# Optimization experiments

Hardware: AMD Instinct MI355X
Metric: run time of the kernel (lower is better)

Reference implementation:

```python
import jax, jax.numpy as jnp
import numpy as np

WINDOWS = (5, 10, 20)
EPS = 1e-4
K_SLICES = 3
OVERLAP = 0.5


def setup_inputs() -> dict:
    key = jax.random.key(0)
    k1, k2, k3, k4 = jax.random.split(key, 4)
    B, T, H = 64, 2048, 256
    x = jax.random.normal(k1, (B, T, H), dtype=jnp.float32)
    alpha = 0.1 * jax.random.normal(k2, (H, len(WINDOWS)), dtype=jnp.float32)
    gamma = 1.0 + 0.1 * jax.random.normal(k3, (K_SLICES, H), dtype=jnp.float32)
    beta = 0.1 * jax.random.normal(k4, (K_SLICES, H), dtype=jnp.float32)
    return {"x": x, "alpha": alpha, "gamma": gamma, "beta": beta}


def _fan(x, alpha):
    # FrequencyAdaptiveNormSimple: multi-window sliding mean/std, blended by softmax(alpha).
    B, T, H = x.shape
    al = jax.nn.softmax(alpha, axis=-1)  # [H, nW]
    # prefix sums for O(T) sliding statistics (same math as unfold mean/std)
    zrow = jnp.zeros((B, 1, H), x.dtype)
    S1 = jnp.concatenate([zrow, jnp.cumsum(x, axis=1)], axis=1)        # [B, T+1, H]
    S2 = jnp.concatenate([zrow, jnp.cumsum(x * x, axis=1)], axis=1)    # [B, T+1, H]
    out = jnp.zeros_like(x)
    for wi, w in enumerate(WINDOWS):
        if w > T:
            continue
        ws = S1[:, w:, :] - S1[:, : T - w + 1, :]    # window sums, [B, T-w+1, H]
        ws2 = S2[:, w:, :] - S2[:, : T - w + 1, :]
        mu = ws / w
        var = jnp.maximum((ws2 - ws * ws / w) / (w - 1), 0.0)  # unbiased (torch std default)
        sd = jnp.maximum(jnp.sqrt(var), EPS)
        # F.pad(..., (w-1, 0), mode='replicate') on the time dim
        mu = jnp.pad(mu, ((0, 0), (w - 1, 0), (0, 0)), mode="edge")
        sd = jnp.pad(sd, ((0, 0), (w - 1, 0), (0, 0)), mode="edge")
        z = jnp.nan_to_num((x - mu) / sd, nan=0.0, posinf=0.0, neginf=0.0)
        out = out + z * al[:, wi][None, None, :]
    return out


def _san(x, gamma, beta):
    # SliceAdaptiveNormSimple: overlapping slices, per-slice (B,T) stats (detached), affine, avg.
    B, T, H = x.shape
    step = max(1, int(round(T / (K_SLICES - (K_SLICES - 1) * OVERLAP))))
    win = min(T, step + int(round(step * OVERLAP)))
    y = jnp.zeros_like(x)
    cnt = jnp.zeros((B, T, 1), x.dtype)
    s = 0
    for k in range(K_SLICES):
        e = min(T, s + win)
        if e <= s:
            break
        xk = x[:, s:e, :]
        mu = jax.lax.stop_gradient(jnp.mean(xk, axis=(0, 1), keepdims=True))
        sd = jax.lax.stop_gradient(
            jnp.maximum(jnp.std(xk, axis=(0, 1), ddof=1, keepdims=True), 1e-4)
        )
        z = jnp.nan_to_num((xk - mu) / sd, nan=0.0, posinf=0.0, neginf=0.0)
        z = z * gamma[k][None, None, :] + beta[k][None, None, :]
        y = y.at[:, s:e, :].add(z)
        cnt = cnt.at[:, s:e, :].add(1.0)
        s += step
    return y / (cnt + EPS)


def reference(x, alpha, gamma, beta):
    # StableFANSAN: out = x + SAN(FAN(x))
    return x + _san(_fan(x, alpha), gamma, beta)
```

## Files before the change

kernel.cpp:

```cpp
#include <hip/hip_runtime.h>
#include <hip/hip_fp16.h>

#define T_DIM 2048
#define H_DIM 256
#define B_DIM 64

#define FCH 64
#define FNCH (T_DIM / FCH)
#define FNCB (B_DIM * FNCH)

#define ECH 64
#define ENCH (T_DIM / ECH)
#define ENCB (B_DIM * ENCH)

#define EPS_F 1e-4f
#define R1 (1.0f / 1.0001f)
#define R2 (1.0f / 2.0001f)

__device__ __forceinline__ void win_stats(float s1, float s2, float inv_w, float inv_wm1,
                                          float& mu, float& isd) {
    mu = s1 * inv_w;
    float var = fmaxf((s2 - s1 * s1 * inv_w) * inv_wm1, 0.0f);
    isd = fminf(rsqrtf(var), 1e4f);
}

template <int MODE, bool FIRST>
__device__ __forceinline__ void run_chunk(
    const float* __restrict__ xbh, __half* __restrict__ s16bh, float* __restrict__ s32bh,
    int t0, float al0, float al1, float al2,
    float& ls1, float& ls2,
    float mu5i, float isd5i, float mu10i, float isd10i, float mu20i, float isd20i) {

    float s1_5 = 0.f, s2_5 = 0.f, s1_10 = 0.f, s2_10 = 0.f, s1_20 = 0.f, s2_20 = 0.f;

    if (!FIRST) {
#pragma unroll
        for (int j = 1; j <= 20; ++j) {
            float v = xbh[(t0 - j) * H_DIM];
            s1_20 += v; s2_20 += v * v;
            if (j <= 10) { s1_10 += v; s2_10 += v * v; }
            if (j <= 5)  { s1_5  += v; s2_5  += v * v; }
        }
    }

    for (int i0 = 0; i0 < FCH; i0 += 32) {
#pragma unroll
        for (int k = 0; k < 32; ++k) {
            const int t = t0 + i0 + k;
            const float v = xbh[t * H_DIM];
            s1_5  += v; s2_5  += v * v;
            s1_10 += v; s2_10 += v * v;
            s1_20 += v; s2_20 += v * v;
            if (!FIRST || i0 + k >= 5)  { float o = xbh[(t - 5)  * H_DIM]; s1_5  -= o; s2_5  -= o * o; }
            if (!FIRST || i0 + k >= 10) { float o = xbh[(t - 10) * H_DIM]; s1_10 -= o; s2_10 -= o * o; }
            if (!FIRST || i0 + k >= 20) { float o = xbh[(t - 20) * H_DIM]; s1_20 -= o; s2_20 -= o * o; }

            float mu, isd, fan = 0.0f;
            if (!FIRST || i0 + k >= 4)  win_stats(s1_5,  s2_5,  0.2f,  0.25f,      mu, isd);
            else { mu = mu5i;  isd = isd5i; }
            fan += (v - mu) * isd * al0;
            if (!FIRST || i0 + k >= 9)  win_stats(s1_10, s2_10, 0.1f,  1.f / 9.f,  mu, isd);
            else { mu = mu10i; isd = isd10i; }
            fan += (v - mu) * isd * al1;
            if (!FIRST || i0 + k >= 19) win_stats(s1_20, s2_20, 0.05f, 1.f / 19.f, mu, isd);
            else { mu = mu20i; isd = isd20i; }
            fan += (v - mu) * isd * al2;

            ls1 += fan; ls2 += fan * fan;
            if (MODE == 0) s16bh[t * H_DIM] = __float2half(fan);
            else           s32bh[t * H_DIM] = fan;
        }
    }
}

template <int MODE>
__global__ __launch_bounds__(256, 4)
void fan_kernel(const float* __restrict__ x, const float* __restrict__ alpha,
                float* __restrict__ part, __half* __restrict__ stash16,
                float* __restrict__ stash32) {
    const int blk = (blockIdx.x & 7) * (FNCB / 8) + (blockIdx.x >> 3);
    const int b = blk / FNCH;
    const int c = blk % FNCH;
    const int h = threadIdx.x;
    const int t0 = c * FCH;
    const size_t base = (size_t)b * T_DIM * H_DIM + h;
    const float* xbh = x + base;
    __half* s16bh = (MODE == 0) ? stash16 + base : nullptr;
    float*  s32bh = (MODE == 1) ? stash32 + base : nullptr;

    const float a0 = alpha[h * 3 + 0], a1 = alpha[h * 3 + 1], a2 = alpha[h * 3 + 2];
    const float mx = fmaxf(a0, fmaxf(a1, a2));
    const float e0 = __expf(a0 - mx), e1 = __expf(a1 - mx), e2 = __expf(a2 - mx);
    const float einv = 1.0f / (e0 + e1 + e2);
    const float al0 = e0 * einv, al1 = e1 * einv, al2 = e2 * einv;

    float ls1 = 0.0f, ls2 = 0.0f;

    if (c == 0) {
        float mu5i, isd5i, mu10i, isd10i, mu20i, isd20i;
        float c1 = 0.f, c2 = 0.f;
#pragma unroll
        for (int j = 0; j < 20; ++j) {
            float v = xbh[j * H_DIM];
            c1 += v; c2 += v * v;
            if (j == 4)  win_stats(c1, c2, 0.2f,  0.25f,      mu5i,  isd5i);
            if (j == 9)  win_stats(c1, c2, 0.1f,  1.f / 9.f,  mu10i, isd10i);
            if (j == 19) win_stats(c1, c2, 0.05f, 1.f / 19.f, mu20i, isd20i);
        }
        run_chunk<MODE, true>(xbh, s16bh, s32bh, t0, al0, al1, al2, ls1, ls2,
                              mu5i, isd5i, mu10i, isd10i, mu20i, isd20i);
    } else {
        run_chunk<MODE, false>(xbh, s16bh, s32bh, t0, al0, al1, al2, ls1, ls2,
                               0.f, 0.f, 0.f, 0.f, 0.f, 0.f);
    }

    part[(0 * FNCB + blk) * H_DIM + h] = ls1;
    part[(1 * FNCB + blk) * H_DIM + h] = ls2;
}

__global__ __launch_bounds__(256)
void reduce_kernel(const float* __restrict__ part, float* __restrict__ acc) {
    const int h = threadIdx.x;
    const int k = blockIdx.x >> 4;
    const int g = blockIdx.x & 15;
    float a1 = 0.f, a2 = 0.f;
    for (int i = 0; i < FNCB / 16; ++i) {
        const int blk = g * (FNCB / 16) + i;
        const int c = blk % FNCH;
        const bool member = (k == 0) ? (c < 24) : (c >= 16);
        if (member) {
            a1 += part[(0 * FNCB + blk) * H_DIM + h];
            a2 += part[(1 * FNCB + blk) * H_DIM + h];
        }
    }
    atomicAdd(&acc[(2 * k)     * H_DIM + h], a1);
    atomicAdd(&acc[(2 * k + 1) * H_DIM + h], a2);
}

__global__ __launch_bounds__(256)
void finalize_kernel(const float* __restrict__ acc, const float* __restrict__ gamma,
                     const float* __restrict__ beta, float* __restrict__ coef) {
    const int h = threadIdx.x;
    const float N0 = 64.0f * 1536.0f, N1 = 64.0f * 1024.0f;
    float S10 = acc[0 * H_DIM + h], S20 = acc[1 * H_DIM + h];
    float S11 = acc[2 * H_DIM + h], S21 = acc[3 * H_DIM + h];
    float mu0 = S10 / N0;
    float v0 = fmaxf((S20 - S10 * S10 / N0) / (N0 - 1.0f), 0.0f);
    float isd0 = 1.0f / fmaxf(sqrtf(v0), EPS_F);
    float mu1 = S11 / N1;
    float v1 = fmaxf((S21 - S11 * S11 / N1) / (N1 - 1.0f), 0.0f);
    float isd1 = 1.0f / fmaxf(sqrtf(v1), EPS_F);
    float A0 = isd0 * gamma[0 * H_DIM + h];
    float A1 = isd1 * gamma[1 * H_DIM + h];
    coef[0 * H_DIM + h] = A0;
    coef[1 * H_DIM + h] = beta[0 * H_DIM + h] - mu0 * A0;
    coef[2 * H_DIM + h] = A1;
    coef[3 * H_DIM + h] = beta[1 * H_DIM + h] - mu1 * A1;
}

template <bool HALF>
__global__ __launch_bounds__(256)
void epilogue_kernel(const float* __restrict__ x, const void* __restrict__ fanp,
                     const float* __restrict__ coef, float* __restrict__ out) {
    const int blk = blockIdx.x;
    const int b = blk / ENCH;
    const int c = blk % ENCH;
    const int wave = threadIdx.x >> 6;
    const int lane = threadIdx.x & 63;
    const int h4 = lane * 4;

    float4 A0 = *(const float4*)&coef[0 * H_DIM + h4];
    float4 B0 = *(const float4*)&coef[1 * H_DIM + h4];
    float4 A1 = *(const float4*)&coef[2 * H_DIM + h4];
    float4 B1 = *(const float4*)&coef[3 * H_DIM + h4];
    float4 A, Bv;
    if (c < 16) {
        A  = make_float4(A0.x * R1, A0.y * R1, A0.z * R1, A0.w * R1);
        Bv = make_float4(B0.x * R1, B0.y * R1, B0.z * R1, B0.w * R1);
    } else if (c >= 24) {
        A  = make_float4(A1.x * R1, A1.y * R1, A1.z * R1, A1.w * R1);
        Bv = make_float4(B1.x * R1, B1.y * R1, B1.z * R1, B1.w * R1);
    } else {
        A  = make_float4((A0.x + A1.x) * R2, (A0.y + A1.y) * R2, (A0.z + A1.z) * R2, (A0.w + A1.w) * R2);
        Bv = make_float4((B0.x + B1.x) * R2, (B0.y + B1.y) * R2, (B0.z + B1.z) * R2, (B0.w + B1.w) * R2);
    }

    const int tbase = c * ECH + wave * 16;
#pragma unroll 4
    for (int i = 0; i < 16; ++i) {
        const size_t idx = ((size_t)b * T_DIM + tbase + i) * H_DIM + h4;
        float4 xv = *(const float4*)&x[idx];
        float4 fv;
        if (HALF) {
            const __half2* fp = (const __half2*)((const __half*)fanp + idx);
            float2 f0 = __half22float2(fp[0]);
            float2 f1 = __half22float2(fp[1]);
            fv = make_float4(f0.x, f0.y, f1.x, f1.y);
        } else {
            fv = *(const float4*)&((const float*)fanp)[idx];
        }
        float4 o;
        o.x = xv.x + fmaf(fv.x, A.x, Bv.x);
        o.y = xv.y + fmaf(fv.y, A.y, Bv.y);
        o.z = xv.z + fmaf(fv.z, A.z, Bv.z);
        o.w = xv.w + fmaf(fv.w, A.w, Bv.w);
        *(float4*)&out[idx] = o;
    }
}

extern "C" void kernel_launch(void* const* d_in, const int* in_sizes, int n_in,
                              void* d_out, int out_size, void* d_ws, size_t ws_size,
                              hipStream_t stream) {
    const float* x     = (const float*)d_in[0];
    const float* alpha = (const float*)d_in[1];
    const float* gamma = (const float*)d_in[2];
    const float* beta  = (const float*)d_in[3];
    float* out  = (float*)d_out;

    float* part = (float*)d_ws;
    float* acc  = part + 2 * FNCB * H_DIM;
    float* coef = acc + 4 * H_DIM;
    __half* stash16 = (__half*)(coef + 4 * H_DIM);
    const size_t need = (size_t)(2 * FNCB * H_DIM + 8 * H_DIM) * 4
                      + (size_t)B_DIM * T_DIM * H_DIM * 2;
    const bool half_path = (ws_size >= need);

    hipMemsetAsync(acc, 0, 4 * H_DIM * sizeof(float), stream);
    if (half_path) {
        fan_kernel<0><<<FNCB, H_DIM, 0, stream>>>(x, alpha, part, stash16, nullptr);
    } else {
        fan_kernel<1><<<FNCB, H_DIM, 0, stream>>>(x, alpha, part, nullptr, out);
    }
    reduce_kernel<<<32, H_DIM, 0, stream>>>(part, acc);
    finalize_kernel<<<1, H_DIM, 0, stream>>>(acc, gamma, beta, coef);
    if (half_path) {
        epilogue_kernel<true><<<ENCB, 256, 0, stream>>>(x, stash16, coef, out);
    } else {
        epilogue_kernel<false><<<ENCB, 256, 0, stream>>>(x, out, coef, out);
    }
}
```

Measured before the change: 373.7 us.

## Pair fp16 stash into half2 time-interleaved layout, register history, fold finalize into epilogue

The FAN kernel keeps a 16-entry register ring of recent x values, so the lag-5 and lag-10 values come from registers rather than repeated global loads. It also writes the fp16 stash as half2 pairs of adjacent timesteps, giving 4-byte stores instead of 2-byte ones. The atomic reduce, memset and finalize kernel are removed: reduce writes partials and each epilogue block recomputes the coefficients into shared memory. The launch-bounds occupancy hint is dropped, which trades possible register spills against occupancy, and every epilogue block now repeats the small coefficient computation.

```diff
diff --git a/kernel.cpp b/kernel.cpp
--- a/kernel.cpp
+++ b/kernel.cpp
@@ -14,8 +14,8 @@
 #define ENCB (B_DIM * ENCH)
 
 #define EPS_F 1e-4f
-#define R1 (1.0f / 1.0001f)
-#define R2 (1.0f / 2.0001f)
+#define R1C (1.0f / 1.0001f)
+#define R2C (1.0f / 2.0001f)
 
 __device__ __forceinline__ void win_stats(float s1, float s2, float inv_w, float inv_wm1,
                                           float& mu, float& isd) {
@@ -26,19 +26,24 @@
 
 template <int MODE, bool FIRST>
 __device__ __forceinline__ void run_chunk(
-    const float* __restrict__ xbh, __half* __restrict__ s16bh, float* __restrict__ s32bh,
+    const float* __restrict__ xbh, __half2* __restrict__ s2bh, float* __restrict__ s32bh,
     int t0, float al0, float al1, float al2,
     float& ls1, float& ls2,
     float mu5i, float isd5i, float mu10i, float isd10i, float mu20i, float isd20i) {
 
     float s1_5 = 0.f, s2_5 = 0.f, s1_10 = 0.f, s2_10 = 0.f, s1_20 = 0.f, s2_20 = 0.f;
-
-    if (!FIRST) {
+    float hist[16];
+    float fprev = 0.0f;
+
+    if (FIRST) {
+#pragma unroll
+        for (int j = 0; j < 16; ++j) hist[j] = 0.0f;
+    } else {
 #pragma unroll
         for (int j = 1; j <= 20; ++j) {
             float v = xbh[(t0 - j) * H_DIM];
             s1_20 += v; s2_20 += v * v;
-            if (j <= 10) { s1_10 += v; s2_10 += v * v; }
+            if (j <= 10) { s1_10 += v; s2_10 += v * v; hist[(16 - j) & 15] = v; }
             if (j <= 5)  { s1_5  += v; s2_5  += v * v; }
         }
     }
@@ -48,12 +53,15 @@
         for (int k = 0; k < 32; ++k) {
             const int t = t0 + i0 + k;
             const float v = xbh[t * H_DIM];
+            float o20 = 0.0f;
+            if (!FIRST || i0 + k >= 20) o20 = xbh[(t - 20) * H_DIM];
             s1_5  += v; s2_5  += v * v;
             s1_10 += v; s2_10 += v * v;
             s1_20 += v; s2_20 += v * v;
-            if (!FIRST || i0 + k >= 5)  { float o = xbh[(t - 5)  * H_DIM]; s1_5  -= o; s2_5  -= o * o; }
-            if (!FIRST || i0 + k >= 10) { float o = xbh[(t - 10) * H_DIM]; s1_10 -= o; s2_10 -= o * o; }
-            if (!FIRST || i0 + k >= 20) { float o = xbh[(t - 20) * H_DIM]; s1_20 -= o; s2_20 -= o * o; }
+            if (!FIRST || i0 + k >= 5)  { float o = hist[(k - 5)  & 15]; s1_5  -= o; s2_5  -= o * o; }
+            if (!FIRST || i0 + k >= 10) { float o = hist[(k - 10) & 15]; s1_10 -= o; s2_10 -= o * o; }
+            if (!FIRST || i0 + k >= 20) { s1_20 -= o20; s2_20 -= o20 * o20; }
+            hist[k & 15] = v;
 
             float mu, isd, fan = 0.0f;
             if (!FIRST || i0 + k >= 4)  win_stats(s1_5,  s2_5,  0.2f,  0.25f,      mu, isd);
@@ -67,14 +75,19 @@
             fan += (v - mu) * isd * al2;
 
             ls1 += fan; ls2 += fan * fan;
-            if (MODE == 0) s16bh[t * H_DIM] = __float2half(fan);
-            else           s32bh[t * H_DIM] = fan;
+            if (MODE == 0) {
+                if (k & 1) s2bh[(size_t)(t >> 1) * H_DIM] =
+                               __halves2half2(__float2half(fprev), __float2half(fan));
+                else       fprev = fan;
+            } else {
+                s32bh[t * H_DIM] = fan;
+            }
         }
     }
 }
 
 template <int MODE>
-__global__ __launch_bounds__(256, 4)
+__global__ __launch_bounds__(256)
 void fan_kernel(const float* __restrict__ x, const float* __restrict__ alpha,
                 float* __restrict__ part, __half* __restrict__ stash16,
                 float* __restrict__ stash32) {
@@ -85,8 +98,9 @@
     const int t0 = c * FCH;
     const size_t base = (size_t)b * T_DIM * H_DIM + h;
     const float* xbh = x + base;
-    __half* s16bh = (MODE == 0) ? stash16 + base : nullptr;
-    float*  s32bh = (MODE == 1) ? stash32 + base : nullptr;
+    __half2* s2bh = (MODE == 0)
+        ? (__half2*)stash16 + (size_t)b * (T_DIM / 2) * H_DIM + h : nullptr;
+    float* s32bh = (MODE == 1) ? stash32 + base : nullptr;
 
     const float a0 = alpha[h * 3 + 0], a1 = alpha[h * 3 + 1], a2 = alpha[h * 3 + 2];
     const float mx = fmaxf(a0, fmaxf(a1, a2));
@@ -107,10 +121,10 @@
             if (j == 9)  win_stats(c1, c2, 0.1f,  1.f / 9.f,  mu10i, isd10i);
             if (j == 19) win_stats(c1, c2, 0.05f, 1.f / 19.f, mu20i, isd20i);
         }
-        run_chunk<MODE, true>(xbh, s16bh, s32bh, t0, al0, al1, al2, ls1, ls2,
+        run_chunk<MODE, true>(xbh, s2bh, s32bh, t0, al0, al1, al2, ls1, ls2,
                               mu5i, isd5i, mu10i, isd10i, mu20i, isd20i);
     } else {
-        run_chunk<MODE, false>(xbh, s16bh, s32bh, t0, al0, al1, al2, ls1, ls2,
+        run_chunk<MODE, false>(xbh, s2bh, s32bh, t0, al0, al1, al2, ls1, ls2,
                                0.f, 0.f, 0.f, 0.f, 0.f, 0.f);
     }
 
@@ -119,7 +133,7 @@
 }
 
 __global__ __launch_bounds__(256)
-void reduce_kernel(const float* __restrict__ part, float* __restrict__ acc) {
+void reduce_kernel(const float* __restrict__ part, float* __restrict__ part2) {
     const int h = threadIdx.x;
     const int k = blockIdx.x >> 4;
     const int g = blockIdx.x & 15;
@@ -133,78 +147,105 @@
             a2 += part[(1 * FNCB + blk) * H_DIM + h];
         }
     }
-    atomicAdd(&acc[(2 * k)     * H_DIM + h], a1);
-    atomicAdd(&acc[(2 * k + 1) * H_DIM + h], a2);
-}
-
-__global__ __launch_bounds__(256)
-void finalize_kernel(const float* __restrict__ acc, const float* __restrict__ gamma,
-                     const float* __restrict__ beta, float* __restrict__ coef) {
-    const int h = threadIdx.x;
-    const float N0 = 64.0f * 1536.0f, N1 = 64.0f * 1024.0f;
-    float S10 = acc[0 * H_DIM + h], S20 = acc[1 * H_DIM + h];
-    float S11 = acc[2 * H_DIM + h], S21 = acc[3 * H_DIM + h];
-    float mu0 = S10 / N0;
-    float v0 = fmaxf((S20 - S10 * S10 / N0) / (N0 - 1.0f), 0.0f);
-    float isd0 = 1.0f / fmaxf(sqrtf(v0), EPS_F);
-    float mu1 = S11 / N1;
-    float v1 = fmaxf((S21 - S11 * S11 / N1) / (N1 - 1.0f), 0.0f);
-    float isd1 = 1.0f / fmaxf(sqrtf(v1), EPS_F);
-    float A0 = isd0 * gamma[0 * H_DIM + h];
-    float A1 = isd1 * gamma[1 * H_DIM + h];
-    coef[0 * H_DIM + h] = A0;
-    coef[1 * H_DIM + h] = beta[0 * H_DIM + h] - mu0 * A0;
-    coef[2 * H_DIM + h] = A1;
-    coef[3 * H_DIM + h] = beta[1 * H_DIM + h] - mu1 * A1;
+    part2[((2 * k + 0) * 16 + g) * H_DIM + h] = a1;
+    part2[((2 * k + 1) * 16 + g) * H_DIM + h] = a2;
 }
 
 template <bool HALF>
 __global__ __launch_bounds__(256)
 void epilogue_kernel(const float* __restrict__ x, const void* __restrict__ fanp,
-                     const float* __restrict__ coef, float* __restrict__ out) {
+                     const float* __restrict__ part2, const float* __restrict__ gamma,
+                     const float* __restrict__ beta, float* __restrict__ out) {
+    __shared__ __align__(16) float cf[4][H_DIM];
+    const int tid = threadIdx.x;
+
+    {
+        float S10 = 0.f, S20 = 0.f, S11 = 0.f, S21 = 0.f;
+#pragma unroll
+        for (int g = 0; g < 16; ++g) {
+            S10 += part2[(0 * 16 + g) * H_DIM + tid];
+            S20 += part2[(1 * 16 + g) * H_DIM + tid];
+            S11 += part2[(2 * 16 + g) * H_DIM + tid];
+            S21 += part2[(3 * 16 + g) * H_DIM + tid];
+        }
+        const float N0 = 64.0f * 1536.0f, N1 = 64.0f * 1024.0f;
+        float mu0 = S10 / N0;
+        float v0 = fmaxf((S20 - S10 * S10 / N0) / (N0 - 1.0f), 0.0f);
+        float isd0 = 1.0f / fmaxf(sqrtf(v0), EPS_F);
+        float mu1 = S11 / N1;
+        float v1 = fmaxf((S21 - S11 * S11 / N1) / (N1 - 1.0f), 0.0f);
+        float isd1 = 1.0f / fmaxf(sqrtf(v1), EPS_F);
+        float A0 = isd0 * gamma[0 * H_DIM + tid];
+        float A1 = isd1 * gamma[1 * H_DIM + tid];
+        cf[0][tid] = A0;
+        cf[1][tid] = beta[0 * H_DIM + tid] - mu0 * A0;
+        cf[2][tid] = A1;
+        cf[3][tid] = beta[1 * H_DIM + tid] - mu1 * A1;
+    }
+    __syncthreads();
+
     const int blk = blockIdx.x;
     const int b = blk / ENCH;
     const int c = blk % ENCH;
-    const int wave = threadIdx.x >> 6;
-    const int lane = threadIdx.x & 63;
+    const int wave = tid >> 6;
+    const int lane = tid & 63;
     const int h4 = lane * 4;
 
-    float4 A0 = *(const float4*)&coef[0 * H_DIM + h4];
-    float4 B0 = *(const float4*)&coef[1 * H_DIM + h4];
-    float4 A1 = *(const float4*)&coef[2 * H_DIM + h4];
-    float4 B1 = *(const float4*)&coef[3 * H_DIM + h4];
+    float4 A0 = *(const float4*)&cf[0][h4];
+    float4 B0 = *(const float4*)&cf[1][h4];
+    float4 A1 = *(const float4*)&cf[2][h4];
+    float4 B1 = *(const float4*)&cf[3][h4];
     float4 A, Bv;
     if (c < 16) {
-        A  = make_float4(A0.x * R1, A0.y * R1, A0.z * R1, A0.w * R1);
-        Bv = make_float4(B0.x * R1, B0.y * R1, B0.z * R1, B0.w * R1);
+        A  = make_float4(A0.x * R1C, A0.y * R1C, A0.z * R1C, A0.w * R1C);
+        Bv = make_float4(B0.x * R1C, B0.y * R1C, B0.z * R1C, B0.w * R1C);
     } else if (c >= 24) {
-        A  = make_float4(A1.x * R1, A1.y * R1, A1.z * R1, A1.w * R1);
-        Bv = make_float4(B1.x * R1, B1.y * R1, B1.z * R1, B1.w * R1);
-    } else {
-        A  = make_float4((A0.x + A1.x) * R2, (A0.y + A1.y) * R2, (A0.z + A1.z) * R2, (A0.w + A1.w) * R2);
-        Bv = make_float4((B0.x + B1.x) * R2, (B0.y + B1.y) * R2, (B0.z + B1.z) * R2, (B0.w + B1.w) * R2);
+        A  = make_float4(A1.x * R1C, A1.y * R1C, A1.z * R1C, A1.w * R1C);
+        Bv = make_float4(B1.x * R1C, B1.y * R1C, B1.z * R1C, B1.w * R1C);
+    } else {
+        A  = make_float4((A0.x + A1.x) * R2C, (A0.y + A1.y) * R2C, (A0.z + A1.z) * R2C, (A0.w + A1.w) * R2C);
+        Bv = make_float4((B0.x + B1.x) * R2C, (B0.y + B1.y) * R2C, (B0.z + B1.z) * R2C, (B0.w + B1.w) * R2C);
     }
 
     const int tbase = c * ECH + wave * 16;
+    if (HALF) {
+        const __half2* s2 = (const __half2*)fanp + (size_t)b * (T_DIM / 2) * H_DIM + h4;
+#pragma unroll 2
+        for (int p = 0; p < 8; ++p) {
+            const int t = tbase + 2 * p;
+            const size_t xi = ((size_t)b * T_DIM + t) * H_DIM + h4;
+            float4 x0 = *(const float4*)&x[xi];
+            float4 x1 = *(const float4*)&x[xi + H_DIM];
+            float4 sv = *(const float4*)(s2 + (size_t)(t >> 1) * H_DIM);
+            __half2 q0 = *reinterpret_cast<const __half2*>(&sv.x);
+            __half2 q1 = *reinterpret_cast<const __half2*>(&sv.y);
+            __half2 q2 = *reinterpret_cast<const __half2*>(&sv.z);
+            __half2 q3 = *reinterpret_cast<const __half2*>(&sv.w);
+            float4 o0, o1;
+            o0.x = x0.x + fmaf(__low2float(q0),  A.x, Bv.x);
+            o0.y = x0.y + fmaf(__low2float(q1),  A.y, Bv.y);
+            o0.z = x0.z + fmaf(__low2float(q2),  A.z, Bv.z);
+            o0.w = x0.w + fmaf(__low2float(q3),  A.w, Bv.w);
+            o1.x = x1.x + fmaf(__high2float(q0), A.x, Bv.x);
+            o1.y = x1.y + fmaf(__high2float(q1), A.y, Bv.y);
+            o1.z = x1.z + fmaf(__high2float(q2), A.z, Bv.z);
+            o1.w = x1.w + fmaf(__high2float(q3), A.w, Bv.w);
+            *(float4*)&out[xi] = o0;
+            *(float4*)&out[xi + H_DIM] = o1;
+        }
+    } else {
 #pragma unroll 4
-    for (int i = 0; i < 16; ++i) {
-        const size_t idx = ((size_t)b * T_DIM + tbase + i) * H_DIM + h4;
-        float4 xv = *(const float4*)&x[idx];
-        float4 fv;
-        if (HALF) {
-            const __half2* fp = (const __half2*)((const __half*)fanp + idx);
-            float2 f0 = __half22float2(fp[0]);
-            float2 f1 = __half22float2(fp[1]);
-            fv = make_float4(f0.x, f0.y, f1.x, f1.y);
-        } else {
-            fv = *(const float4*)&((const float*)fanp)[idx];
-        }
-        float4 o;
-        o.x = xv.x + fmaf(fv.x, A.x, Bv.x);
-        o.y = xv.y + fmaf(fv.y, A.y, Bv.y);
-        o.z = xv.z + fmaf(fv.z, A.z, Bv.z);
-        o.w = xv.w + fmaf(fv.w, A.w, Bv.w);
-        *(float4*)&out[idx] = o;
+        for (int i = 0; i < 16; ++i) {
+            const size_t idx = ((size_t)b * T_DIM + tbase + i) * H_DIM + h4;
+            float4 xv = *(const float4*)&x[idx];
+            float4 fv = *(const float4*)&((const float*)fanp)[idx];
+            float4 o;
+            o.x = xv.x + fmaf(fv.x, A.x, Bv.x);
+            o.y = xv.y + fmaf(fv.y, A.y, Bv.y);
+            o.z = xv.z + fmaf(fv.z, A.z, Bv.z);
+            o.w = xv.w + fmaf(fv.w, A.w, Bv.w);
+            *(float4*)&out[idx] = o;
+        }
     }
 }
 
@@ -217,25 +258,22 @@
     const float* beta  = (const float*)d_in[3];
     float* out  = (float*)d_out;
 
-    float* part = (float*)d_ws;
-    float* acc  = part + 2 * FNCB * H_DIM;
-    float* coef = acc + 4 * H_DIM;
-    __half* stash16 = (__half*)(coef + 4 * H_DIM);
-    const size_t need = (size_t)(2 * FNCB * H_DIM + 8 * H_DIM) * 4
+    float* part  = (float*)d_ws;
+    float* part2 = part + 2 * FNCB * H_DIM;
+    __half* stash16 = (__half*)(part2 + 64 * H_DIM);
+    const size_t need = (size_t)(2 * FNCB * H_DIM + 64 * H_DIM) * 4
                       + (size_t)B_DIM * T_DIM * H_DIM * 2;
     const bool half_path = (ws_size >= need);
 
-    hipMemsetAsync(acc, 0, 4 * H_DIM * sizeof(float), stream);
     if (half_path) {
         fan_kernel<0><<<FNCB, H_DIM, 0, stream>>>(x, alpha, part, stash16, nullptr);
     } else {
         fan_kernel<1><<<FNCB, H_DIM, 0, stream>>>(x, alpha, part, nullptr, out);
     }
-    reduce_kernel<<<32, H_DIM, 0, stream>>>(part, acc);
-    finalize_kernel<<<1, H_DIM, 0, stream>>>(acc, gamma, beta, coef);
+    reduce_kernel<<<32, H_DIM, 0, stream>>>(part, part2);
     if (half_path) {
-        epilogue_kernel<true><<<ENCB, 256, 0, stream>>>(x, stash16, coef, out);
-    } else {
-        epilogue_kernel<false><<<ENCB, 256, 0, stream>>>(x, out, coef, out);
-    }
-}
+        epilogue_kernel<true><<<ENCB, 256, 0, stream>>>(x, stash16, part2, gamma, beta, out);
+    } else {
+        epilogue_kernel<false><<<ENCB, 256, 0, stream>>>(x, out, part2, gamma, beta, out);
+    }
+}
```

Result: faster. 352.3 us (-5.7%).
